# Kernel tuning notes

Measured on AMD Instinct MI355X. Metric: run time of the kernel, lower is better.

Reference implementation:

```python
import jax, jax.numpy as jnp
import numpy as np

C64 = jnp.complex64

# ---- gate matrices (PennyLane conventions) ----

def u3(theta, phi, delta):
    ct, st = jnp.cos(theta / 2), jnp.sin(theta / 2)
    return jnp.stack([
        jnp.stack([ct + 0j, -jnp.exp(1j * delta) * st]),
        jnp.stack([jnp.exp(1j * phi) * st, jnp.exp(1j * (phi + delta)) * ct]),
    ]).astype(C64)

def ising_zz(t):
    em, ep = jnp.exp(-1j * t / 2), jnp.exp(1j * t / 2)
    return jnp.diag(jnp.stack([em, ep, ep, em])).astype(C64)

_XX = np.fliplr(np.eye(4)).astype(np.complex64)
_YY = np.array([[0, 0, 0, -1], [0, 0, 1, 0], [0, 1, 0, 0], [-1, 0, 0, 0]], np.complex64)
_I4 = np.eye(4, dtype=np.complex64)

def ising_xx(t):
    return (jnp.cos(t / 2) * _I4 - 1j * jnp.sin(t / 2) * _XX).astype(C64)

def ising_yy(t):
    return (jnp.cos(t / 2) * _I4 - 1j * jnp.sin(t / 2) * _YY).astype(C64)

def crot(phi, theta, omega):
    # controlled-Rot(phi,theta,omega); control = first wire of apply_2q
    ct, st = jnp.cos(theta / 2), jnp.sin(theta / 2)
    r = jnp.stack([
        jnp.stack([jnp.exp(-1j * (phi + omega) / 2) * ct, -jnp.exp(1j * (phi - omega) / 2) * st]),
        jnp.stack([jnp.exp(-1j * (phi - omega) / 2) * st, jnp.exp(1j * (phi + omega) / 2) * ct]),
    ])
    U = jnp.eye(4, dtype=C64)
    return U.at[2:, 2:].set(r.astype(C64))

# ---- statevector gate application; state shape (S, 2, 2, ..., 2) (wire 0 = axis 1) ----

def apply_1q(state, U, q):
    st = jnp.tensordot(U, state, axes=[[1], [q + 1]])  # (2, S, ...)
    return jnp.moveaxis(st, 0, q + 1)

def apply_2q(state, U4, q1, q2):
    Ut = U4.reshape(2, 2, 2, 2)  # (o1, o2, i1, i2)
    st = jnp.tensordot(Ut, state, axes=[[2, 3], [q1 + 1, q2 + 1]])
    return jnp.moveaxis(st, [0, 1], [q1 + 1, q2 + 1])

KERNEL, DILATION = 8, 1

def setup_inputs() -> dict:
    key = jax.random.key(0)
    ks = jax.random.split(key, 5)
    B, C, T = 16, 32, 128
    nq, depth = 10, 3
    return {
        "x": jax.random.normal(ks[0], (B, C, T), jnp.float32),
        "fc_w": jax.random.normal(ks[1], (nq, C * KERNEL), jnp.float32) * (1.0 / np.sqrt(C * KERNEL)),
        "fc_b": jax.random.normal(ks[2], (nq,), jnp.float32) * 0.01,
        "conv_params": jax.random.normal(ks[3], (depth, nq, 15), jnp.float32),
        "pool_params": jax.random.normal(ks[4], (depth, nq // 2, 3), jnp.float32),
    }

def reference(x, fc_w, fc_b, conv_params, pool_params):
    B, C, T = x.shape
    nq = fc_w.shape[0]
    k = fc_w.shape[1] // C
    depth = conv_params.shape[0]
    d = DILATION
    n_win = T - (k - 1) * d

    # temporal windows -> classical embedding (angles)
    idx = jnp.arange(n_win)[:, None] + d * jnp.arange(k)[None, :]  # (n_win, k)
    win = x[:, :, idx]                                             # (B, C, n_win, k)
    flat = jnp.transpose(win, (0, 2, 1, 3)).reshape(B, n_win, C * k)
    angles = (jnp.einsum('bwf,ef->bwe', flat, fc_w) + fc_b).reshape(-1, nq)  # (S, nq)
    S = angles.shape[0]

    # AngleEmbedding with RY on |0...0> gives a product state
    half = angles / 2
    c, s = jnp.cos(half), jnp.sin(half)
    state = jnp.ones((S, 1), C64)
    for q in range(nq):
        qubit = jnp.stack([c[:, q], s[:, q]], axis=-1).astype(C64)  # (S, 2)
        state = (state[:, :, None] * qubit[:, None, :]).reshape(S, -1)
    state = state.reshape((S,) + (2,) * nq)

    wires = list(range(nq))
    for layer in range(depth):
        W = conv_params[layer]
        P = pool_params[layer]
        nw = len(wires)
        # convolution: U3 pairs + IsingZZ/YY/XX + U3 pairs, even then odd brickwork
        for p in (0, 1):
            for indx in range(nw - 1):
                if indx % 2 == p:
                    w1, w2 = wires[indx], wires[indx + 1]
                    state = apply_1q(state, u3(*W[indx, 0:3]), w1)
                    state = apply_1q(state, u3(*W[indx + 1, 3:6]), w2)
                    state = apply_2q(state, ising_zz(W[indx, 6]), w1, w2)
                    state = apply_2q(state, ising_yy(W[indx, 7]), w1, w2)
                    state = apply_2q(state, ising_xx(W[indx, 8]), w1, w2)
                    state = apply_1q(state, u3(*W[indx, 9:12]), w1)
                    state = apply_1q(state, u3(*W[indx + 1, 12:15]), w2)
        # pooling: CRot from discarded (odd) wire onto kept (even) wire
        for j in range(nw // 2):
            ctrl, tgt = wires[2 * j + 1], wires[2 * j]
            state = apply_2q(state, crot(*P[j]), ctrl, tgt)
        wires = wires[::2]

    # expval(PauliZ(0))
    probs = state.real ** 2 + state.imag ** 2
    p01 = probs.reshape(S, 2, -1).sum(-1)  # marginal over wire 0
    z = p01[:, 0] - p01[:, 1]
    return z.reshape(B, n_win)
```

## Files before the change

### kernel.cpp

```cpp
#include <hip/hip_runtime.h>

#define NWIN 121
#define NQ 10
#define NGATES 23
#define WPB 4

typedef float v2f __attribute__((ext_vector_type(2)));

static constexpr int GT [NGATES] = {0,0,0,0,0,0,0,0,0, 1,1,1,1,1, 0,0,0,0, 1,1, 0,0, 1};
static constexpr int GL [NGATES] = {0,0,0,0,0,0,0,0,0, 0,0,0,0,0, 1,1,1,1, 1,1, 2,2, 2};
static constexpr int GP [NGATES] = {0,2,4,6,8,1,3,5,7, 0,1,2,3,4, 0,2,1,3, 0,1, 0,1, 0};
__device__ static const int dGT[NGATES] = {0,0,0,0,0,0,0,0,0, 1,1,1,1,1, 0,0,0,0, 1,1, 0,0, 1};
__device__ static const int dGL[NGATES] = {0,0,0,0,0,0,0,0,0, 0,0,0,0,0, 1,1,1,1, 1,1, 2,2, 2};
__device__ static const int dGP[NGATES] = {0,2,4,6,8,1,3,5,7, 0,1,2,3,4, 0,2,1,3, 0,1, 0,1, 0};

__host__ __device__ constexpr int REGB[6][4] = {
    {5,6,7,8},{1,2,3,4},{4,5,8,9},{0,1,3,5},{3,5,7,9},{0,1,5,9}};
__host__ __device__ constexpr int LANEB[6][6] = {
    {0,1,2,3,4,9},{0,5,6,7,8,9},{0,1,2,3,6,7},
    {2,4,6,7,8,9},{0,1,2,4,6,8},{2,3,4,6,7,8}};

__host__ __device__ constexpr int hswz(int p, int L){
    return p==0 ? ((((L>>5)&1)<<1)|(((L>>6)&1)<<2)|(((L>>7)&1)<<3))
         : p==1 ? ((((L>>6)&1)<<1)|(((L>>7)&1)<<2)|(((L>>8)&1)<<3))
         : p==2 ? (((L>>4)&1)|(((L>>6)&1)<<1)|(((L>>7)&1)<<3))
         :        (((L>>4)&1)|(((L>>6)&1)<<1)|(((L>>8)&1)<<3));
}
__host__ __device__ constexpr int offsL(int ph, int r){
    int o = 0;
    for (int k=0;k<4;++k) if ((r>>k)&1) o |= 1<<REGB[ph][k];
    return o;
}

struct cpx { float x, y; };
__device__ __forceinline__ cpx cmul(cpx a, cpx b){ return {a.x*b.x - a.y*b.y, a.x*b.y + a.y*b.x}; }
__device__ __forceinline__ cpx cadd(cpx a, cpx b){ return {a.x+b.x, a.y+b.y}; }
__device__ __forceinline__ cpx cscale(float s, cpx a){ return {s*a.x, s*a.y}; }
__device__ __forceinline__ cpx cexp_i(float t){ return {cosf(t), sinf(t)}; }
__device__ __forceinline__ cpx mulnegi(cpx z){ return {z.y, -z.x}; }

__device__ __forceinline__ void u3m(cpx A[2][2], float th, float ph, float de){
    float ct = cosf(0.5f*th), st = sinf(0.5f*th);
    cpx ed  = cexp_i(de);
    cpx ep  = cexp_i(ph);
    cpx epd = cexp_i(ph + de);
    A[0][0] = {ct, 0.f};
    A[0][1] = {-ed.x*st, -ed.y*st};
    A[1][0] = { ep.x*st,  ep.y*st};
    A[1][1] = { epd.x*ct, epd.y*ct};
}

__device__ __forceinline__ void build_gate(int g, const float* __restrict__ conv,
                                           const float* __restrict__ pool,
                                           cpx (&M)[4][4])
{
    int l = dGL[g], pi = dGP[g];
    if (dGT[g] == 0) {
        const float* W1 = conv + l*150 + pi*15;
        const float* W2 = conv + l*150 + (pi+1)*15;
        cpx A1[2][2], B1[2][2], A2[2][2], B2[2][2];
        u3m(A1, W1[0],  W1[1],  W1[2]);
        u3m(B1, W2[3],  W2[4],  W2[5]);
        u3m(A2, W1[9],  W1[10], W1[11]);
        u3m(B2, W2[12], W2[13], W2[14]);
        cpx T[4][4];
        #pragma unroll
        for (int r1=0;r1<2;++r1)
        #pragma unroll
        for (int r2=0;r2<2;++r2)
        #pragma unroll
        for (int c1=0;c1<2;++c1)
        #pragma unroll
        for (int c2=0;c2<2;++c2)
            T[2*r1+r2][2*c1+c2] = cmul(A1[r1][c1], B1[r2][c2]);
        float tz = W1[6];
        cpx em = cexp_i(-0.5f*tz), ep = cexp_i(0.5f*tz);
        cpx dz[4] = {em, ep, ep, em};
        #pragma unroll
        for (int r=0;r<4;++r)
        #pragma unroll
        for (int c=0;c<4;++c) T[r][c] = cmul(dz[r], T[r][c]);
        float ty = W1[7]; float cy = cosf(0.5f*ty), sy = sinf(0.5f*ty);
        cpx T2_[4][4];
        #pragma unroll
        for (int c=0;c<4;++c) {
            T2_[0][c] = cadd(cscale(cy,T[0][c]), mulnegi(cscale(-sy, T[3][c])));
            T2_[1][c] = cadd(cscale(cy,T[1][c]), mulnegi(cscale( sy, T[2][c])));
            T2_[2][c] = cadd(cscale(cy,T[2][c]), mulnegi(cscale( sy, T[1][c])));
            T2_[3][c] = cadd(cscale(cy,T[3][c]), mulnegi(cscale(-sy, T[0][c])));
        }
        float tx = W1[8]; float cx = cosf(0.5f*tx), sx = sinf(0.5f*tx);
        cpx T3_[4][4];
        #pragma unroll
        for (int c=0;c<4;++c) {
            T3_[0][c] = cadd(cscale(cx,T2_[0][c]), mulnegi(cscale(sx, T2_[3][c])));
            T3_[1][c] = cadd(cscale(cx,T2_[1][c]), mulnegi(cscale(sx, T2_[2][c])));
            T3_[2][c] = cadd(cscale(cx,T2_[2][c]), mulnegi(cscale(sx, T2_[1][c])));
            T3_[3][c] = cadd(cscale(cx,T2_[3][c]), mulnegi(cscale(sx, T2_[0][c])));
        }
        cpx K2[4][4];
        #pragma unroll
        for (int r1=0;r1<2;++r1)
        #pragma unroll
        for (int r2=0;r2<2;++r2)
        #pragma unroll
        for (int c1=0;c1<2;++c1)
        #pragma unroll
        for (int c2=0;c2<2;++c2)
            K2[2*r1+r2][2*c1+c2] = cmul(A2[r1][c1], B2[r2][c2]);
        #pragma unroll
        for (int r=0;r<4;++r)
        #pragma unroll
        for (int c=0;c<4;++c) {
            cpx acc = {0.f, 0.f};
            #pragma unroll
            for (int m=0;m<4;++m) acc = cadd(acc, cmul(K2[r][m], T3_[m][c]));
            M[r][c] = acc;
        }
    } else {
        const float* Pp = pool + l*15 + pi*3;
        float phi = Pp[0], th = Pp[1], om = Pp[2];
        float ct = cosf(0.5f*th), st = sinf(0.5f*th);
        #pragma unroll
        for (int r=0;r<4;++r)
        #pragma unroll
        for (int c=0;c<4;++c) M[r][c] = {0.f, 0.f};
        M[0][0] = {1.f, 0.f};
        M[1][1] = {1.f, 0.f};
        M[2][2] = cscale( ct, cexp_i(-0.5f*(phi+om)));
        M[2][3] = cscale(-st, cexp_i( 0.5f*(phi-om)));
        M[3][2] = cscale( st, cexp_i(-0.5f*(phi-om)));
        M[3][3] = cscale( ct, cexp_i( 0.5f*(phi+om)));
    }
}


__device__ __forceinline__ v2f cfma(v2f m, v2f v, v2f acc) {
    v2f sw = {v.y, v.x};
    v2f my = {-m.y, m.y};
    v2f t = __builtin_elementwise_fma(my, sw, acc);
    v2f mx = {m.x, m.x};
    return __builtin_elementwise_fma(mx, v, t);
}
__device__ __forceinline__ v2f cmulv(v2f a, v2f b) { return cfma(a, b, (v2f){0.f,0.f}); }
__device__ __forceinline__ v2f vsel(int c, v2f a, v2f b) {
    return (v2f){ c ? a.x : b.x, c ? a.y : b.y };
}

__device__ __forceinline__ void wave_lds_fence() {
    asm volatile("s_waitcnt lgkmcnt(0)" ::: "memory");
}

template<int P1, int P2>
__device__ __forceinline__ void gate4(v2f (&st)[16], const float2* __restrict__ g) {
    v2f m[16];
    #pragma unroll
    for (int k = 0; k < 16; ++k) { float2 t = g[k]; m[k] = (v2f){t.x, t.y}; }
    constexpr int M1 = 1 << P1, M2 = 1 << P2;
    #pragma unroll
    for (int b = 0; b < 16; ++b) {
        if (b & (M1 | M2)) continue;
        v2f v0 = st[b], v1 = st[b|M2], v2 = st[b|M1], v3 = st[b|M1|M2];
        #pragma unroll
        for (int row = 0; row < 4; ++row) {
            v2f acc = cfma(m[row*4+0], v0, (v2f){0.f, 0.f});
            acc = cfma(m[row*4+1], v1, acc);
            acc = cfma(m[row*4+2], v2, acc);
            acc = cfma(m[row*4+3], v3, acc);
            st[b | ((row>>1) ? M1 : 0) | ((row&1) ? M2 : 0)] = acc;
        }
    }
}

template<int P1, int P2>
__device__ __forceinline__ void crot4(v2f (&st)[16], const float2* __restrict__ g) {
    float2 t;
    t = g[10]; v2f m22 = {t.x, t.y};
    t = g[11]; v2f m23 = {t.x, t.y};
    t = g[14]; v2f m32 = {t.x, t.y};
    t = g[15]; v2f m33 = {t.x, t.y};
    constexpr int M1 = 1 << P1, M2 = 1 << P2;
    #pragma unroll
    for (int b = 0; b < 16; ++b) {
        if (!(b & M1) || (b & M2)) continue;
        v2f v2_ = st[b], v3_ = st[b|M2];
        st[b]    = cfma(m23, v3_, cfma(m22, v2_, (v2f){0.f,0.f}));
        st[b|M2] = cfma(m33, v3_, cfma(m32, v2_, (v2f){0.f,0.f}));
    }
}

template<int PH>
__device__ __forceinline__ int base_of(int lane) {
    int b = 0;
    #pragma unroll
    for (int j = 0; j < 6; ++j) b |= ((lane >> j) & 1) << LANEB[PH][j];
    return b;
}

template<int PERM>
__device__ __forceinline__ void permute(v2f (&st)[16], char* lds, int lane) {
    int bw0 = base_of<PERM>(lane);
    int bw = (bw0 ^ hswz(PERM, bw0)) << 3;
    #pragma unroll
    for (int r = 0; r < 16; ++r) {
        const int o = offsL(PERM, r);
        const int C = (o ^ hswz(PERM, o)) << 3;
        *reinterpret_cast<v2f*>(lds + (bw ^ C)) = st[r];
    }
    wave_lds_fence();
    int br0 = base_of<PERM+1>(lane);
    int br = (br0 ^ hswz(PERM, br0)) << 3;
    #pragma unroll
    for (int r = 0; r < 16; ++r) {
        const int o = offsL(PERM+1, r);
        const int C = (o ^ hswz(PERM, o)) << 3;
        st[r] = *reinterpret_cast<const v2f*>(lds + (br ^ C));
    }
    wave_lds_fence();
}

__global__ __launch_bounds__(256) void hqtcn_fused(
    const float* __restrict__ x,
    const float* __restrict__ fc_w,
    const float* __restrict__ fc_b,
    const float* __restrict__ conv,
    const float* __restrict__ pool,
    float* __restrict__ out)
{
    __shared__ float2 gmat[NGATES*16];
    __shared__ float2 pbuf[WPB][1024];

    const int tid  = threadIdx.x;
    const int wid  = tid >> 6;
    const int lane = tid & 63;
    const int s = blockIdx.x * WPB + wid;
    const int b = s / NWIN, w = s % NWIN;
    char* lds = reinterpret_cast<char*>(&pbuf[wid][0]);

    float xv[4];
    #pragma unroll
    for (int j = 0; j < 4; ++j) {
        int f = lane + 64*j;
        xv[j] = x[b*4096 + (f >> 3)*128 + w + (f & 7)];
    }
    float cq[NQ], sq[NQ];
    #pragma unroll
    for (int e = 0; e < NQ; ++e) {
        float v = 0.f;
        #pragma unroll
        for (int j = 0; j < 4; ++j)
            v = fmaf(xv[j], fc_w[e*256 + lane + 64*j], v);
        #pragma unroll
        for (int off = 32; off >= 1; off >>= 1) v += __shfl_xor(v, off);
        float h = 0.5f * (v + fc_b[e]);
        __sincosf(h, &sq[e], &cq[e]);
    }

    if (tid < NGATES) {
        cpx M[4][4];
        build_gate(tid, conv, pool, M);
        #pragma unroll
        for (int r = 0; r < 4; ++r)
        #pragma unroll
        for (int c = 0; c < 4; ++c)
            gmat[tid*16 + r*4 + c] = make_float2(M[r][c].x, M[r][c].y);
    }
    __syncthreads();

    v2f W[5][4];
    #pragma unroll
    for (int p = 0; p < 5; ++p) {
        float ca = cq[2*p], sa = sq[2*p], cb = cq[2*p+1], sb = sq[2*p+1];
        float u0 = ca*cb, u1 = ca*sb, u2 = sa*cb, u3_ = sa*sb;
        const float2* G = gmat + p*16;
        #pragma unroll
        for (int i = 0; i < 4; ++i) {
            float2 g0 = G[i*4+0], g1 = G[i*4+1], g2 = G[i*4+2], g3 = G[i*4+3];
            v2f acc = (v2f){g0.x*u0, g0.y*u0};
            acc = __builtin_elementwise_fma((v2f){u1,u1}, (v2f){g1.x,g1.y}, acc);
            acc = __builtin_elementwise_fma((v2f){u2,u2}, (v2f){g2.x,g2.y}, acc);
            acc = __builtin_elementwise_fma((v2f){u3_,u3_}, (v2f){g3.x,g3.y}, acc);
            W[p][i] = acc;
        }
    }
    const int l0 = lane&1, l1=(lane>>1)&1, l2=(lane>>2)&1,
              l3=(lane>>3)&1, l4=(lane>>4)&1, l5=(lane>>5)&1;
    v2f W3k = vsel(l3, vsel(l2, W[3][3], W[3][2]), vsel(l2, W[3][1], W[3][0]));
    v2f W4k = vsel(l1, vsel(l0, W[4][3], W[4][2]), vsel(l0, W[4][1], W[4][0]));
    v2f UL  = cmulv(W3k, W4k);
    v2f W2lo = vsel(l4, W[2][1], W[2][0]);
    v2f W2hi = vsel(l4, W[2][3], W[2][2]);
    v2f P0 = cmulv(UL, vsel(l5, W[0][2], W[0][0]));
    v2f P1 = cmulv(UL, vsel(l5, W[0][3], W[0][1]));
    v2f PW[2][4];
    #pragma unroll
    for (int j = 0; j < 4; ++j) {
        PW[0][j] = cmulv(P0, W[1][j]);
        PW[1][j] = cmulv(P1, W[1][j]);
    }
    v2f st[16];
    #pragma unroll
    for (int r = 0; r < 16; ++r)
        st[r] = cmulv(PW[(r>>3)&1][(r>>1)&3], (r&1) ? W2hi : W2lo);

    const float2* gm = gmat;

    gate4<3,2>(st, gm + 5*16);
    gate4<1,0>(st, gm + 6*16);
    crot4<1,2>(st, gm + 10*16);
    permute<0>(st, lds, lane);
    gate4<3,2>(st, gm + 7*16);
    gate4<1,0>(st, gm + 8*16);
    crot4<1,2>(st, gm + 12*16);
    permute<1>(st, lds, lane);
    crot4<2,3>(st, gm + 9*16);
    crot4<0,1>(st, gm + 11*16);
    permute<2>(st, lds, lane);
    crot4<0,1>(st, gm + 13*16);
    gate4<3,2>(st, gm + 15*16);
    gate4<2,1>(st, gm + 17*16);
    permute<3>(st, lds, lane);
    gate4<3,2>(st, gm + 14*16);
    gate4<2,1>(st, gm + 16*16);
    crot4<2,3>(st, gm + 18*16);
    crot4<0,1>(st, gm + 19*16);
    permute<4>(st, lds, lane);
    gate4<3,2>(st, gm + 20*16);
    gate4<2,1>(st, gm + 21*16);
    crot4<2,3>(st, gm + 22*16);

    float accp = 0.f, accm = 0.f;
    #pragma unroll
    for (int r = 0; r < 16; ++r) {
        v2f a = st[r];
        float p2 = fmaf(a.x, a.x, a.y*a.y);
        if ((r >> 3) & 1) accm += p2; else accp += p2;
    }
    float acc = accp - accm;
    #pragma unroll
    for (int off = 32; off >= 1; off >>= 1) acc += __shfl_xor(acc, off);
    if (lane == 0) out[s] = acc;
}

extern "C" void kernel_launch(void* const* d_in, const int* in_sizes, int n_in,
                              void* d_out, int out_size, void* d_ws, size_t ws_size,
                              hipStream_t stream) {
    const float* x     = (const float*)d_in[0];
    const float* fc_w  = (const float*)d_in[1];
    const float* fc_b  = (const float*)d_in[2];
    const float* convp = (const float*)d_in[3];
    const float* poolp = (const float*)d_in[4];
    float* out = (float*)d_out;

    hqtcn_fused<<<(16*NWIN)/WPB, 64*WPB, 0, stream>>>(x, fc_w, fc_b, convp, poolp, out);
}
```

Measured before the change: 27.91 us.

## Cut LDS permutes via shuffle-based cross-lane gates, double-buffer, parallel gate build

Reworks the statevector qubit-to-register/lane mapping so it needs three LDS permutes instead of five. Some gates that span a lane bit are now applied with cross-lane shuffles (crotx, gate4x). Alternate permutes write to ping-pong LDS buffers, so the trailing wait after each permute is dropped. Gate matrices are built column-wise by 92 threads instead of 23, and this work moves before the FC reduction. Gate matrices are loaded with float4 reads and prefetched ahead of the permutes. In exchange the new swizzle and mapping logic is more intricate and could be wrong, and the added shuffles have their own cost.

```diff
diff --git a/kernel.cpp b/kernel.cpp
--- a/kernel.cpp
+++ b/kernel.cpp
@@ -7,24 +7,19 @@
 
 typedef float v2f __attribute__((ext_vector_type(2)));
 
-static constexpr int GT [NGATES] = {0,0,0,0,0,0,0,0,0, 1,1,1,1,1, 0,0,0,0, 1,1, 0,0, 1};
-static constexpr int GL [NGATES] = {0,0,0,0,0,0,0,0,0, 0,0,0,0,0, 1,1,1,1, 1,1, 2,2, 2};
-static constexpr int GP [NGATES] = {0,2,4,6,8,1,3,5,7, 0,1,2,3,4, 0,2,1,3, 0,1, 0,1, 0};
 __device__ static const int dGT[NGATES] = {0,0,0,0,0,0,0,0,0, 1,1,1,1,1, 0,0,0,0, 1,1, 0,0, 1};
 __device__ static const int dGL[NGATES] = {0,0,0,0,0,0,0,0,0, 0,0,0,0,0, 1,1,1,1, 1,1, 2,2, 2};
 __device__ static const int dGP[NGATES] = {0,2,4,6,8,1,3,5,7, 0,1,2,3,4, 0,2,1,3, 0,1, 0,1, 0};
 
-__host__ __device__ constexpr int REGB[6][4] = {
-    {5,6,7,8},{1,2,3,4},{4,5,8,9},{0,1,3,5},{3,5,7,9},{0,1,5,9}};
-__host__ __device__ constexpr int LANEB[6][6] = {
-    {0,1,2,3,4,9},{0,5,6,7,8,9},{0,1,2,3,6,7},
-    {2,4,6,7,8,9},{0,1,2,4,6,8},{2,3,4,6,7,8}};
+__host__ __device__ constexpr int REGB[4][4] = {
+    {5,6,7,8},{1,2,3,4},{0,1,3,5},{3,5,7,9}};
+__host__ __device__ constexpr int LANEB[4][6] = {
+    {0,1,2,3,4,9},{0,5,6,7,8,9},{2,4,6,7,8,9},{0,1,2,4,6,8}};
 
 __host__ __device__ constexpr int hswz(int p, int L){
     return p==0 ? ((((L>>5)&1)<<1)|(((L>>6)&1)<<2)|(((L>>7)&1)<<3))
-         : p==1 ? ((((L>>6)&1)<<1)|(((L>>7)&1)<<2)|(((L>>8)&1)<<3))
-         : p==2 ? (((L>>4)&1)|(((L>>6)&1)<<1)|(((L>>7)&1)<<3))
-         :        (((L>>4)&1)|(((L>>6)&1)<<1)|(((L>>8)&1)<<3));
+         : p==1 ? (((L>>4)&1) | ((((L>>5)&1)^((L>>6)&1))<<1) | (((L>>7)&1)<<2) | (((L>>8)&1)<<3))
+         :        (((L>>4)&1) | (((L>>6)&1)<<1) | (((L>>8)&1)<<3));
 }
 __host__ __device__ constexpr int offsL(int ph, int r){
     int o = 0;
@@ -50,9 +45,10 @@
     A[1][1] = { epd.x*ct, epd.y*ct};
 }
 
-__device__ __forceinline__ void build_gate(int g, const float* __restrict__ conv,
-                                           const float* __restrict__ pool,
-                                           cpx (&M)[4][4])
+__device__ __forceinline__ void build_gate_col(int g, int c,
+                                               const float* __restrict__ conv,
+                                               const float* __restrict__ pool,
+                                               cpx (&Mc)[4])
 {
     int l = dGL[g], pi = dGP[g];
     if (dGT[g] == 0) {
@@ -63,74 +59,58 @@
         u3m(B1, W2[3],  W2[4],  W2[5]);
         u3m(A2, W1[9],  W1[10], W1[11]);
         u3m(B2, W2[12], W2[13], W2[14]);
-        cpx T[4][4];
+        const int c1 = c >> 1, c2 = c & 1;
+        cpx T[4];
         #pragma unroll
         for (int r1=0;r1<2;++r1)
         #pragma unroll
         for (int r2=0;r2<2;++r2)
-        #pragma unroll
-        for (int c1=0;c1<2;++c1)
-        #pragma unroll
-        for (int c2=0;c2<2;++c2)
-            T[2*r1+r2][2*c1+c2] = cmul(A1[r1][c1], B1[r2][c2]);
+            T[2*r1+r2] = cmul(A1[r1][c1], B1[r2][c2]);
         float tz = W1[6];
         cpx em = cexp_i(-0.5f*tz), ep = cexp_i(0.5f*tz);
-        cpx dz[4] = {em, ep, ep, em};
-        #pragma unroll
-        for (int r=0;r<4;++r)
-        #pragma unroll
-        for (int c=0;c<4;++c) T[r][c] = cmul(dz[r], T[r][c]);
+        T[0] = cmul(em, T[0]); T[1] = cmul(ep, T[1]);
+        T[2] = cmul(ep, T[2]); T[3] = cmul(em, T[3]);
         float ty = W1[7]; float cy = cosf(0.5f*ty), sy = sinf(0.5f*ty);
-        cpx T2_[4][4];
-        #pragma unroll
-        for (int c=0;c<4;++c) {
-            T2_[0][c] = cadd(cscale(cy,T[0][c]), mulnegi(cscale(-sy, T[3][c])));
-            T2_[1][c] = cadd(cscale(cy,T[1][c]), mulnegi(cscale( sy, T[2][c])));
-            T2_[2][c] = cadd(cscale(cy,T[2][c]), mulnegi(cscale( sy, T[1][c])));
-            T2_[3][c] = cadd(cscale(cy,T[3][c]), mulnegi(cscale(-sy, T[0][c])));
-        }
+        cpx T2_[4];
+        T2_[0] = cadd(cscale(cy,T[0]), mulnegi(cscale(-sy, T[3])));
+        T2_[1] = cadd(cscale(cy,T[1]), mulnegi(cscale( sy, T[2])));
+        T2_[2] = cadd(cscale(cy,T[2]), mulnegi(cscale( sy, T[1])));
+        T2_[3] = cadd(cscale(cy,T[3]), mulnegi(cscale(-sy, T[0])));
         float tx = W1[8]; float cx = cosf(0.5f*tx), sx = sinf(0.5f*tx);
-        cpx T3_[4][4];
-        #pragma unroll
-        for (int c=0;c<4;++c) {
-            T3_[0][c] = cadd(cscale(cx,T2_[0][c]), mulnegi(cscale(sx, T2_[3][c])));
-            T3_[1][c] = cadd(cscale(cx,T2_[1][c]), mulnegi(cscale(sx, T2_[2][c])));
-            T3_[2][c] = cadd(cscale(cx,T2_[2][c]), mulnegi(cscale(sx, T2_[1][c])));
-            T3_[3][c] = cadd(cscale(cx,T2_[3][c]), mulnegi(cscale(sx, T2_[0][c])));
-        }
+        cpx T3_[4];
+        T3_[0] = cadd(cscale(cx,T2_[0]), mulnegi(cscale(sx, T2_[3])));
+        T3_[1] = cadd(cscale(cx,T2_[1]), mulnegi(cscale(sx, T2_[2])));
+        T3_[2] = cadd(cscale(cx,T2_[2]), mulnegi(cscale(sx, T2_[1])));
+        T3_[3] = cadd(cscale(cx,T2_[3]), mulnegi(cscale(sx, T2_[0])));
         cpx K2[4][4];
         #pragma unroll
         for (int r1=0;r1<2;++r1)
         #pragma unroll
         for (int r2=0;r2<2;++r2)
         #pragma unroll
-        for (int c1=0;c1<2;++c1)
-        #pragma unroll
-        for (int c2=0;c2<2;++c2)
-            K2[2*r1+r2][2*c1+c2] = cmul(A2[r1][c1], B2[r2][c2]);
-        #pragma unroll
-        for (int r=0;r<4;++r)
-        #pragma unroll
-        for (int c=0;c<4;++c) {
+        for (int d1=0;d1<2;++d1)
+        #pragma unroll
+        for (int d2=0;d2<2;++d2)
+            K2[2*r1+r2][2*d1+d2] = cmul(A2[r1][d1], B2[r2][d2]);
+        #pragma unroll
+        for (int r=0;r<4;++r) {
             cpx acc = {0.f, 0.f};
             #pragma unroll
-            for (int m=0;m<4;++m) acc = cadd(acc, cmul(K2[r][m], T3_[m][c]));
-            M[r][c] = acc;
+            for (int m=0;m<4;++m) acc = cadd(acc, cmul(K2[r][m], T3_[m]));
+            Mc[r] = acc;
         }
     } else {
         const float* Pp = pool + l*15 + pi*3;
         float phi = Pp[0], th = Pp[1], om = Pp[2];
         float ct = cosf(0.5f*th), st = sinf(0.5f*th);
         #pragma unroll
-        for (int r=0;r<4;++r)
-        #pragma unroll
-        for (int c=0;c<4;++c) M[r][c] = {0.f, 0.f};
-        M[0][0] = {1.f, 0.f};
-        M[1][1] = {1.f, 0.f};
-        M[2][2] = cscale( ct, cexp_i(-0.5f*(phi+om)));
-        M[2][3] = cscale(-st, cexp_i( 0.5f*(phi-om)));
-        M[3][2] = cscale( st, cexp_i(-0.5f*(phi-om)));
-        M[3][3] = cscale( ct, cexp_i( 0.5f*(phi+om)));
+        for (int r=0;r<4;++r) Mc[r] = {0.f, 0.f};
+        if (c == 0) Mc[0] = {1.f, 0.f};
+        if (c == 1) Mc[1] = {1.f, 0.f};
+        if (c == 2) { Mc[2] = cscale( ct, cexp_i(-0.5f*(phi+om)));
+                      Mc[3] = cscale( st, cexp_i(-0.5f*(phi-om))); }
+        if (c == 3) { Mc[2] = cscale(-st, cexp_i( 0.5f*(phi-om)));
+                      Mc[3] = cscale( ct, cexp_i( 0.5f*(phi+om))); }
     }
 }
 
@@ -151,11 +131,24 @@
     asm volatile("s_waitcnt lgkmcnt(0)" ::: "memory");
 }
 
+__device__ __forceinline__ void load16(const float2* __restrict__ g, v2f (&m)[16]) {
+    const float4* g4 = reinterpret_cast<const float4*>(g);
+    #pragma unroll
+    for (int k = 0; k < 8; ++k) {
+        float4 t = g4[k];
+        m[2*k]   = (v2f){t.x, t.y};
+        m[2*k+1] = (v2f){t.z, t.w};
+    }
+}
+__device__ __forceinline__ void load4(const float2* __restrict__ g, v2f (&c4)[4]) {
+    const float4* g4 = reinterpret_cast<const float4*>(g);
+    float4 a = g4[5], b = g4[7];
+    c4[0] = (v2f){a.x,a.y}; c4[1] = (v2f){a.z,a.w};
+    c4[2] = (v2f){b.x,b.y}; c4[3] = (v2f){b.z,b.w};
+}
+
 template<int P1, int P2>
-__device__ __forceinline__ void gate4(v2f (&st)[16], const float2* __restrict__ g) {
-    v2f m[16];
-    #pragma unroll
-    for (int k = 0; k < 16; ++k) { float2 t = g[k]; m[k] = (v2f){t.x, t.y}; }
+__device__ __forceinline__ void gate4m(v2f (&st)[16], const v2f (&m)[16]) {
     constexpr int M1 = 1 << P1, M2 = 1 << P2;
     #pragma unroll
     for (int b = 0; b < 16; ++b) {
@@ -173,19 +166,54 @@
 }
 
 template<int P1, int P2>
-__device__ __forceinline__ void crot4(v2f (&st)[16], const float2* __restrict__ g) {
-    float2 t;
-    t = g[10]; v2f m22 = {t.x, t.y};
-    t = g[11]; v2f m23 = {t.x, t.y};
-    t = g[14]; v2f m32 = {t.x, t.y};
-    t = g[15]; v2f m33 = {t.x, t.y};
+__device__ __forceinline__ void crot4m(v2f (&st)[16], const v2f (&c4)[4]) {
     constexpr int M1 = 1 << P1, M2 = 1 << P2;
     #pragma unroll
     for (int b = 0; b < 16; ++b) {
         if (!(b & M1) || (b & M2)) continue;
         v2f v2_ = st[b], v3_ = st[b|M2];
-        st[b]    = cfma(m23, v3_, cfma(m22, v2_, (v2f){0.f,0.f}));
-        st[b|M2] = cfma(m33, v3_, cfma(m32, v2_, (v2f){0.f,0.f}));
+        st[b]    = cfma(c4[1], v3_, cmulv(c4[0], v2_));
+        st[b|M2] = cfma(c4[3], v3_, cmulv(c4[2], v2_));
+    }
+}
+
+template<int PCTRL, int LBIT>
+__device__ __forceinline__ void crotx(v2f (&st)[16], const v2f (&c4)[4], int lane) {
+    const int beta = (lane >> LBIT) & 1;
+    v2f S0 = vsel(beta, c4[3], c4[0]);
+    v2f S1 = vsel(beta, c4[2], c4[1]);
+    constexpr int M1 = 1 << PCTRL;
+    #pragma unroll
+    for (int b = 0; b < 16; ++b) {
+        if (!(b & M1)) continue;
+        v2f u = st[b], p;
+        p.x = __shfl_xor(u.x, 1 << LBIT);
+        p.y = __shfl_xor(u.y, 1 << LBIT);
+        st[b] = cfma(S1, p, cmulv(S0, u));
+    }
+}
+
+template<int PREG, int LBIT>
+__device__ __forceinline__ void gate4x(v2f (&st)[16], const v2f (&m)[16], int lane) {
+    const int beta = (lane >> LBIT) & 1;
+    v2f A00 = vsel(beta, m[5],  m[0]);
+    v2f A01 = vsel(beta, m[4],  m[1]);
+    v2f A02 = vsel(beta, m[7],  m[2]);
+    v2f A03 = vsel(beta, m[6],  m[3]);
+    v2f A10 = vsel(beta, m[13], m[8]);
+    v2f A11 = vsel(beta, m[12], m[9]);
+    v2f A12 = vsel(beta, m[15], m[10]);
+    v2f A13 = vsel(beta, m[14], m[11]);
+    constexpr int M1 = 1 << PREG;
+    #pragma unroll
+    for (int b = 0; b < 16; ++b) {
+        if (b & M1) continue;
+        v2f u0 = st[b], u1 = st[b|M1], p0, p1;
+        p0.x = __shfl_xor(u0.x, 1 << LBIT); p0.y = __shfl_xor(u0.y, 1 << LBIT);
+        p1.x = __shfl_xor(u1.x, 1 << LBIT); p1.y = __shfl_xor(u1.y, 1 << LBIT);
+        v2f r0 = cfma(A03, p1, cfma(A02, u1, cfma(A01, p0, cmulv(A00, u0))));
+        v2f r1 = cfma(A13, p1, cfma(A12, u1, cfma(A11, p0, cmulv(A10, u0))));
+        st[b] = r0; st[b|M1] = r1;
     }
 }
 
@@ -197,26 +225,25 @@
     return b;
 }
 
-template<int PERM>
-__device__ __forceinline__ void permute(v2f (&st)[16], char* lds, int lane) {
-    int bw0 = base_of<PERM>(lane);
-    int bw = (bw0 ^ hswz(PERM, bw0)) << 3;
+template<int P>
+__device__ __forceinline__ void permute(v2f (&st)[16], char* buf, int lane) {
+    int bw0 = base_of<P>(lane);
+    int bw = (bw0 ^ hswz(P, bw0)) << 3;
     #pragma unroll
     for (int r = 0; r < 16; ++r) {
-        const int o = offsL(PERM, r);
-        const int C = (o ^ hswz(PERM, o)) << 3;
-        *reinterpret_cast<v2f*>(lds + (bw ^ C)) = st[r];
+        const int o = offsL(P, r);
+        const int C = (o ^ hswz(P, o)) << 3;
+        *reinterpret_cast<v2f*>(buf + (bw ^ C)) = st[r];
     }
     wave_lds_fence();
-    int br0 = base_of<PERM+1>(lane);
-    int br = (br0 ^ hswz(PERM, br0)) << 3;
+    int br0 = base_of<P+1>(lane);
+    int br = (br0 ^ hswz(P, br0)) << 3;
     #pragma unroll
     for (int r = 0; r < 16; ++r) {
-        const int o = offsL(PERM+1, r);
-        const int C = (o ^ hswz(PERM, o)) << 3;
-        st[r] = *reinterpret_cast<const v2f*>(lds + (br ^ C));
-    }
-    wave_lds_fence();
+        const int o = offsL(P+1, r);
+        const int C = (o ^ hswz(P, o)) << 3;
+        st[r] = *reinterpret_cast<const v2f*>(buf + (br ^ C));
+    }
 }
 
 __global__ __launch_bounds__(256) void hqtcn_fused(
@@ -228,14 +255,13 @@
     float* __restrict__ out)
 {
     __shared__ float2 gmat[NGATES*16];
-    __shared__ float2 pbuf[WPB][1024];
+    __shared__ float2 pbuf[WPB][2][1024];
 
     const int tid  = threadIdx.x;
     const int wid  = tid >> 6;
     const int lane = tid & 63;
     const int s = blockIdx.x * WPB + wid;
     const int b = s / NWIN, w = s % NWIN;
-    char* lds = reinterpret_cast<char*>(&pbuf[wid][0]);
 
     float xv[4];
     #pragma unroll
@@ -243,6 +269,15 @@
         int f = lane + 64*j;
         xv[j] = x[b*4096 + (f >> 3)*128 + w + (f & 7)];
     }
+
+    if (tid < 4*NGATES) {
+        cpx Mc[4];
+        build_gate_col(tid >> 2, tid & 3, conv, pool, Mc);
+        #pragma unroll
+        for (int r = 0; r < 4; ++r)
+            gmat[(tid>>2)*16 + r*4 + (tid&3)] = make_float2(Mc[r].x, Mc[r].y);
+    }
+
     float cq[NQ], sq[NQ];
     #pragma unroll
     for (int e = 0; e < NQ; ++e) {
@@ -254,16 +289,6 @@
         for (int off = 32; off >= 1; off >>= 1) v += __shfl_xor(v, off);
         float h = 0.5f * (v + fc_b[e]);
         __sincosf(h, &sq[e], &cq[e]);
-    }
-
-    if (tid < NGATES) {
-        cpx M[4][4];
-        build_gate(tid, conv, pool, M);
-        #pragma unroll
-        for (int r = 0; r < 4; ++r)
-        #pragma unroll
-        for (int c = 0; c < 4; ++c)
-            gmat[tid*16 + r*4 + c] = make_float2(M[r][c].x, M[r][c].y);
     }
     __syncthreads();
 
@@ -290,13 +315,13 @@
     v2f UL  = cmulv(W3k, W4k);
     v2f W2lo = vsel(l4, W[2][1], W[2][0]);
     v2f W2hi = vsel(l4, W[2][3], W[2][2]);
-    v2f P0 = cmulv(UL, vsel(l5, W[0][2], W[0][0]));
-    v2f P1 = cmulv(UL, vsel(l5, W[0][3], W[0][1]));
+    v2f P0v = cmulv(UL, vsel(l5, W[0][2], W[0][0]));
+    v2f P1v = cmulv(UL, vsel(l5, W[0][3], W[0][1]));
     v2f PW[2][4];
     #pragma unroll
     for (int j = 0; j < 4; ++j) {
-        PW[0][j] = cmulv(P0, W[1][j]);
-        PW[1][j] = cmulv(P1, W[1][j]);
+        PW[0][j] = cmulv(P0v, W[1][j]);
+        PW[1][j] = cmulv(P1v, W[1][j]);
     }
     v2f st[16];
     #pragma unroll
@@ -304,30 +329,32 @@
         st[r] = cmulv(PW[(r>>3)&1][(r>>1)&3], (r&1) ? W2hi : W2lo);
 
     const float2* gm = gmat;
-
-    gate4<3,2>(st, gm + 5*16);
-    gate4<1,0>(st, gm + 6*16);
-    crot4<1,2>(st, gm + 10*16);
-    permute<0>(st, lds, lane);
-    gate4<3,2>(st, gm + 7*16);
-    gate4<1,0>(st, gm + 8*16);
-    crot4<1,2>(st, gm + 12*16);
-    permute<1>(st, lds, lane);
-    crot4<2,3>(st, gm + 9*16);
-    crot4<0,1>(st, gm + 11*16);
-    permute<2>(st, lds, lane);
-    crot4<0,1>(st, gm + 13*16);
-    gate4<3,2>(st, gm + 15*16);
-    gate4<2,1>(st, gm + 17*16);
-    permute<3>(st, lds, lane);
-    gate4<3,2>(st, gm + 14*16);
-    gate4<2,1>(st, gm + 16*16);
-    crot4<2,3>(st, gm + 18*16);
-    crot4<0,1>(st, gm + 19*16);
-    permute<4>(st, lds, lane);
-    gate4<3,2>(st, gm + 20*16);
-    gate4<2,1>(st, gm + 21*16);
-    crot4<2,3>(st, gm + 22*16);
+    v2f m[16], pm[16], c4[4], pc4[4];
+
+    load16(gm + 5*16, m);   gate4m<3,2>(st, m);
+    load16(gm + 6*16, m);   gate4m<1,0>(st, m);
+    load4 (gm + 10*16, c4); crot4m<1,2>(st, c4);
+    load4 (gm +  9*16, c4); crotx<3,5>(st, c4, lane);
+    load16(gm + 7*16, pm);
+    permute<0>(st, (char*)&pbuf[wid][0][0], lane);
+    gate4m<3,2>(st, pm);
+    load16(gm + 8*16, m);   gate4m<1,0>(st, m);
+    load4 (gm + 12*16, c4); crot4m<1,2>(st, c4);
+    load4 (gm + 11*16, c4); crotx<3,1>(st, c4, lane);
+    load4 (gm + 13*16, pc4);
+    permute<1>(st, (char*)&pbuf[wid][1][0], lane);
+    crot4m<0,1>(st, pc4);
+    load16(gm + 15*16, m);  gate4m<3,2>(st, m);
+    load16(gm + 17*16, m);  gate4m<2,1>(st, m);
+    load16(gm + 14*16, pm);
+    permute<2>(st, (char*)&pbuf[wid][0][0], lane);
+    gate4m<3,2>(st, pm);
+    load16(gm + 16*16, m);  gate4m<2,1>(st, m);
+    load4 (gm + 18*16, c4); crot4m<2,3>(st, c4);
+    load4 (gm + 19*16, c4); crot4m<0,1>(st, c4);
+    load16(gm + 20*16, m);  gate4m<3,1>(st, m);
+    load16(gm + 21*16, m);  gate4x<1,1>(st, m, lane);
+    load4 (gm + 22*16, c4); crot4m<1,3>(st, c4);
 
     float accp = 0.f, accm = 0.f;
     #pragma unroll
```

New measurement: 39.01 us. 1.4x slower.
